# Optimization experiments

Hardware: AMD Instinct MI355X
Metric: run time of the kernel (lower is better)

The kernel has to match this reference:

```python
import jax, jax.numpy as jnp
import numpy as np

N, C, K, D = 65536, 64, 16, 2
EPS = 1e-5


def batch_norm(x, g, b):
    # training-mode BatchNorm1d over rows (biased variance), x: [rows, C]
    m = x.mean(axis=0)
    v = ((x - m) ** 2).mean(axis=0)
    return (x - m) * jax.lax.rsqrt(v + EPS) * g + b


def setup_inputs() -> dict:
    key = jax.random.key(0)
    ks = jax.random.split(key, 20)
    s = 1.0 / np.sqrt(C)
    inp = {
        "coord": jax.random.normal(ks[0], (N, 3), jnp.float32),
        "feat": jax.random.normal(ks[1], (N, C), jnp.float32),
        "reference_index": jax.random.randint(ks[2], (N, K), 0, N, jnp.int32),
        # per-block stacked params, leading dim D
        "fc1_w": jax.random.uniform(ks[3], (D, C, C), jnp.float32, -s, s),
        "bn1_g": jnp.ones((D, C), jnp.float32),
        "bn1_b": jnp.zeros((D, C), jnp.float32),
        "la_w1": jax.random.uniform(ks[4], (D, C, C), jnp.float32, -s, s),
        "la_b1": jax.random.uniform(ks[5], (D, C), jnp.float32, -s, s),
        "la_bn1_g": jnp.ones((D, C), jnp.float32),
        "la_bn1_b": jnp.zeros((D, C), jnp.float32),
        "la_w2": jax.random.uniform(ks[6], (D, C, C), jnp.float32, -s, s),
        "la_b2": jax.random.uniform(ks[7], (D, C), jnp.float32, -s, s),
        "la_bn2_g": jnp.ones((D, C), jnp.float32),
        "la_bn2_b": jnp.zeros((D, C), jnp.float32),
        "fc3_w": jax.random.uniform(ks[8], (D, C, C), jnp.float32, -s, s),
        "bn2_g": jnp.ones((D, C), jnp.float32),
        "bn2_b": jnp.zeros((D, C), jnp.float32),
        "bn3_g": jnp.ones((D, C), jnp.float32),
        "bn3_b": jnp.zeros((D, C), jnp.float32),
    }
    return inp


def reference(coord, feat, reference_index,
              fc1_w, bn1_g, bn1_b,
              la_w1, la_b1, la_bn1_g, la_bn1_b,
              la_w2, la_b2, la_bn2_g, la_bn2_b,
              fc3_w, bn2_g, bn2_b, bn3_g, bn3_b):
    ref = reference_index  # [n, k]
    for d in range(D):
        identity = feat
        # fc1 (no bias) -> bn1 -> relu
        x = jax.nn.relu(batch_norm(feat @ fc1_w[d].T, bn1_g[d], bn1_b[d]))
        # LocalAggregation: gather neighbors, shared MLP on [n*k, c], max over k
        grouped = x[ref].reshape(-1, C)                      # [n*k, c]
        h = jax.nn.relu(batch_norm(grouped @ la_w1[d].T + la_b1[d],
                                   la_bn1_g[d], la_bn1_b[d]))
        h = jax.nn.relu(batch_norm(h @ la_w2[d].T + la_b2[d],
                                   la_bn2_g[d], la_bn2_b[d]))
        x = h.reshape(ref.shape[0], K, C).max(axis=1)        # [n, c]
        # bn2 -> relu -> fc3 (no bias) -> bn3
        x = jax.nn.relu(batch_norm(x, bn2_g[d], bn2_b[d]))
        x = batch_norm(x @ fc3_w[d].T, bn3_g[d], bn3_b[d])
        feat = jax.nn.relu(identity + x)
    return feat
```

## Files before the change

kernel.cpp:

```cpp
#include <hip/hip_runtime.h>

#define N_PTS 65536
#define BN_EPS 1e-5f
#define NSHD 64
#define NSB  (10 * NSHD * 128)

typedef __attribute__((ext_vector_type(8))) short bf16x8;
typedef __attribute__((ext_vector_type(4))) float f32x4;

static __device__ __forceinline__ unsigned short f2bf(float f) {
    unsigned u = __builtin_bit_cast(unsigned, f);
    u += 0x7fffu + ((u >> 16) & 1u);
    return (unsigned short)(u >> 16);
}
static __device__ __forceinline__ float bf2f(unsigned short h) {
    unsigned u = ((unsigned)h) << 16;
    return __builtin_bit_cast(float, u);
}
static __device__ __forceinline__ unsigned pack2(float a, float b) {
    return (unsigned)f2bf(a) | ((unsigned)f2bf(b) << 16);
}

template<int PRE, int BIAS, int WTD, int OUTBF, int INBF, int HIST>
__global__ __launch_bounds__(256, 4) void mm_kernel(
    const void*  __restrict__ inv_,  const float* __restrict__ identity,
    const float* __restrict__ Wg,    const float* __restrict__ bias,
    const float* __restrict__ gg,    const float* __restrict__ bb,
    const float* __restrict__ S_in,  float inv_denom,
    void*        __restrict__ outv,  float* __restrict__ S_out,
    const unsigned* __restrict__ cw, float* __restrict__ f1_out,
    const int* __restrict__ ref,     unsigned* __restrict__ hdst)
{
    __shared__ unsigned short lwh[64][72], lwl[64][72];
    __shared__ float stg[4][16][68];
    __shared__ float sc[64], sh[64];
    __shared__ float LS[4][64], LQ[4][64];
    float* PS = &stg[0][0][0];

    const int tid  = threadIdx.x;
    const int lane = tid & 63, wid = tid >> 6;
    const int l15  = lane & 15, kg = lane >> 4;
    const int brow = blockIdx.x * 64;
    const int arow = brow + wid * 16 + l15;

    const int wr = tid >> 2, wc = (tid & 3) * 16;
    const float4* wp = (const float4*)(Wg + wr * 64 + wc);
    float4 wv0 = wp[0], wv1 = wp[1], wv2 = wp[2], wv3 = wp[3];

    float xv[2][8];
    uint4 ub0, ub1;
    float4 a0, a1, a2, a3;
    if (INBF) {
        const uint4* ap = (const uint4*)((const unsigned*)inv_ +
                                         (size_t)arow * 32 + kg * 4);
        ub0 = ap[0]; ub1 = ap[4];
    } else {
        const float4* ap = (const float4*)((const float*)inv_ +
                                           (size_t)arow * 64 + kg * 8);
        a0 = ap[0]; a1 = ap[1]; a2 = ap[8]; a3 = ap[9];
    }
    float4 i0, i1, i2, i3;
    if (PRE == 2) {
        const float4* ip = (const float4*)(identity + (size_t)arow * 64 + kg * 8);
        i0 = ip[0]; i1 = ip[1]; i2 = ip[8]; i3 = ip[9];
    }
    uint4 cc;
    if (WTD) cc = ((const uint4*)(cw + brow + wid * 16))[kg];
    if (HIST) {
        int4 hv = ((const int4*)(ref + brow * 16))[tid];
        atomicAdd(&hdst[hv.x], 1u); atomicAdd(&hdst[hv.y], 1u);
        atomicAdd(&hdst[hv.z], 1u); atomicAdd(&hdst[hv.w], 1u);
    }

    {
        float wf[16] = {wv0.x,wv0.y,wv0.z,wv0.w, wv1.x,wv1.y,wv1.z,wv1.w,
                        wv2.x,wv2.y,wv2.z,wv2.w, wv3.x,wv3.y,wv3.z,wv3.w};
        unsigned ph[8], pl[8];
        #pragma unroll
        for (int q = 0; q < 8; ++q) {
            unsigned short h0 = f2bf(wf[2*q]),   h1 = f2bf(wf[2*q+1]);
            unsigned short l0 = f2bf(wf[2*q]   - bf2f(h0));
            unsigned short l1 = f2bf(wf[2*q+1] - bf2f(h1));
            ph[q] = (unsigned)h0 | ((unsigned)h1 << 16);
            pl[q] = (unsigned)l0 | ((unsigned)l1 << 16);
        }
        uint4* dh = (uint4*)(&lwh[wr][wc]);
        uint4* dl = (uint4*)(&lwl[wr][wc]);
        dh[0] = make_uint4(ph[0], ph[1], ph[2], ph[3]);
        dh[1] = make_uint4(ph[4], ph[5], ph[6], ph[7]);
        dl[0] = make_uint4(pl[0], pl[1], pl[2], pl[3]);
        dl[1] = make_uint4(pl[4], pl[5], pl[6], pl[7]);
    }

    if (PRE >= 1) {
        const int idx = tid & 127, hh = tid >> 7;
        float acc = 0.f;
        #pragma unroll
        for (int g = 0; g < NSHD / 2; ++g)
            acc += S_in[(hh * (NSHD / 2) + g) * 128 + idx];
        PS[hh * 128 + idx] = acc;
        __syncthreads();
        if (tid < 128) PS[tid] += PS[128 + tid];
        __syncthreads();
        if (tid < 64) {
            float s = PS[tid], q = PS[64 + tid];
            float m   = s * inv_denom;
            float var = q * inv_denom - m * m;
            float scl = gg[tid] * rsqrtf(var + BN_EPS);
            sc[tid] = scl; sh[tid] = bb[tid] - m * scl;
        }
    }
    __syncthreads();

    if (INBF) {
        uint4 uu[2] = {ub0, ub1};
        #pragma unroll
        for (int ks = 0; ks < 2; ++ks) {
            unsigned w0 = uu[ks].x, w1 = uu[ks].y, w2 = uu[ks].z, w3 = uu[ks].w;
            xv[ks][0] = bf2f((unsigned short)(w0 & 0xffffu));
            xv[ks][1] = bf2f((unsigned short)(w0 >> 16));
            xv[ks][2] = bf2f((unsigned short)(w1 & 0xffffu));
            xv[ks][3] = bf2f((unsigned short)(w1 >> 16));
            xv[ks][4] = bf2f((unsigned short)(w2 & 0xffffu));
            xv[ks][5] = bf2f((unsigned short)(w2 >> 16));
            xv[ks][6] = bf2f((unsigned short)(w3 & 0xffffu));
            xv[ks][7] = bf2f((unsigned short)(w3 >> 16));
        }
    } else {
        xv[0][0]=a0.x; xv[0][1]=a0.y; xv[0][2]=a0.z; xv[0][3]=a0.w;
        xv[0][4]=a1.x; xv[0][5]=a1.y; xv[0][6]=a1.z; xv[0][7]=a1.w;
        xv[1][0]=a2.x; xv[1][1]=a2.y; xv[1][2]=a2.z; xv[1][3]=a2.w;
        xv[1][4]=a3.x; xv[1][5]=a3.y; xv[1][6]=a3.z; xv[1][7]=a3.w;
    }

    if (PRE == 1) {
        #pragma unroll
        for (int ks = 0; ks < 2; ++ks)
            #pragma unroll
            for (int j = 0; j < 8; ++j) {
                int k = ks * 32 + kg * 8 + j;
                xv[ks][j] = fmaxf(xv[ks][j] * sc[k] + sh[k], 0.f);
            }
    } else if (PRE == 2) {
        float idv[2][8];
        idv[0][0]=i0.x; idv[0][1]=i0.y; idv[0][2]=i0.z; idv[0][3]=i0.w;
        idv[0][4]=i1.x; idv[0][5]=i1.y; idv[0][6]=i1.z; idv[0][7]=i1.w;
        idv[1][0]=i2.x; idv[1][1]=i2.y; idv[1][2]=i2.z; idv[1][3]=i2.w;
        idv[1][4]=i3.x; idv[1][5]=i3.y; idv[1][6]=i3.z; idv[1][7]=i3.w;
        #pragma unroll
        for (int ks = 0; ks < 2; ++ks) {
            #pragma unroll
            for (int j = 0; j < 8; ++j) {
                int k = ks * 32 + kg * 8 + j;
                xv[ks][j] = fmaxf(idv[ks][j] + xv[ks][j] * sc[k] + sh[k], 0.f);
            }
            float* f1p = f1_out + (size_t)arow * 64 + kg * 8 + ks * 32;
            *(float4*)(f1p)     = make_float4(xv[ks][0], xv[ks][1], xv[ks][2], xv[ks][3]);
            *(float4*)(f1p + 4) = make_float4(xv[ks][4], xv[ks][5], xv[ks][6], xv[ks][7]);
        }
    }

    bf16x8 ahi[2], alo[2];
    #pragma unroll
    for (int ks = 0; ks < 2; ++ks) {
        bf16x8 th, tl;
        #pragma unroll
        for (int j = 0; j < 8; ++j) {
            unsigned short h = f2bf(xv[ks][j]);
            th[j] = (short)h;
            tl[j] = (short)f2bf(xv[ks][j] - bf2f(h));
        }
        ahi[ks] = th; alo[ks] = tl;
    }
    f32x4 d[4];
    #pragma unroll
    for (int ct = 0; ct < 4; ++ct) {
        float bc = BIAS ? bias[ct * 16 + l15] : 0.f;
        d[ct] = (f32x4){bc, bc, bc, bc};
    }
    #pragma unroll
    for (int ct = 0; ct < 4; ++ct) {
        const int gcol = ct * 16 + l15;
        #pragma unroll
        for (int ks = 0; ks < 2; ++ks) {
            bf16x8 wh = *(const bf16x8*)(&lwh[gcol][ks * 32 + kg * 8]);
            bf16x8 wl = *(const bf16x8*)(&lwl[gcol][ks * 32 + kg * 8]);
            d[ct] = __builtin_amdgcn_mfma_f32_16x16x32_bf16(ahi[ks], wh, d[ct], 0, 0, 0);
            d[ct] = __builtin_amdgcn_mfma_f32_16x16x32_bf16(alo[ks], wh, d[ct], 0, 0, 0);
            d[ct] = __builtin_amdgcn_mfma_f32_16x16x32_bf16(ahi[ks], wl, d[ct], 0, 0, 0);
        }
    }

    float wt[4] = {1.f, 1.f, 1.f, 1.f};
    if (WTD) {
        wt[0] = (float)cc.x; wt[1] = (float)cc.y;
        wt[2] = (float)cc.z; wt[3] = (float)cc.w;
    }
    float ts[4], tq[4];
    #pragma unroll
    for (int ct = 0; ct < 4; ++ct) {
        float t = 0.f, t2 = 0.f;
        #pragma unroll
        for (int i = 0; i < 4; ++i) {
            float v = d[ct][i];
            t += wt[i] * v; t2 += wt[i] * v * v;
        }
        ts[ct] = t; tq[ct] = t2;
    }

    #pragma unroll
    for (int ct = 0; ct < 4; ++ct)
        #pragma unroll
        for (int i = 0; i < 4; ++i)
            stg[wid][kg * 4 + i][ct * 16 + l15] = d[ct][i];
    __syncthreads();
    if (!OUTBF) {
        float* op = (float*)outv + (size_t)arow * 64 + kg * 16;
        const float* srow = &stg[wid][l15][kg * 16];
        *(float4*)(op + 0)  = *(const float4*)(srow + 0);
        *(float4*)(op + 4)  = *(const float4*)(srow + 4);
        *(float4*)(op + 8)  = *(const float4*)(srow + 8);
        *(float4*)(op + 12) = *(const float4*)(srow + 12);
    } else {
        const float* srow = &stg[wid][l15][kg * 16];
        unsigned pk[8];
        #pragma unroll
        for (int q = 0; q < 8; ++q) pk[q] = pack2(srow[2 * q], srow[2 * q + 1]);
        unsigned* op = (unsigned*)outv;
        uint4* dst = (uint4*)(op + (size_t)arow * 32 + kg * 8);
        dst[0] = make_uint4(pk[0], pk[1], pk[2], pk[3]);
        dst[1] = make_uint4(pk[4], pk[5], pk[6], pk[7]);
    }

    #pragma unroll
    for (int ct = 0; ct < 4; ++ct) {
        float a = ts[ct], b = tq[ct];
        a += __shfl_xor(a, 16);  a += __shfl_xor(a, 32);
        b += __shfl_xor(b, 16);  b += __shfl_xor(b, 32);
        if (kg == 0) { LS[wid][ct * 16 + l15] = a; LQ[wid][ct * 16 + l15] = b; }
    }
    __syncthreads();
    const int bsel = blockIdx.x & (NSHD - 1);
    if (tid < 64)
        atomicAdd(S_out + bsel * 128 + tid,
                  LS[0][tid] + LS[1][tid] + LS[2][tid] + LS[3][tid]);
    else if (tid < 128) {
        int c = tid - 64;
        atomicAdd(S_out + bsel * 128 + 64 + c,
                  LQ[0][c] + LQ[1][c] + LQ[2][c] + LQ[3][c]);
    }
}

__global__ __launch_bounds__(256) void gather_kernel(
    const unsigned* __restrict__ y3u, const int* __restrict__ ref,
    const float* __restrict__ S_in, float inv_denom,
    const float* __restrict__ gg, const float* __restrict__ bb,
    unsigned* __restrict__ xmu, float* __restrict__ S_out)
{
    __shared__ float scs[64], shs[64], Rs[256], Rq[256], PS[256];
    const int tid = threadIdx.x;
    const int lane = tid & 63, wid = tid >> 6;
    const int c2 = lane & 31;
    const int hsel = lane & 32;
    const int p0 = blockIdx.x * 8 + wid * 2;
    const int r0 = 2 * p0 + (hsel ? 1 : 0);
    const int r1 = r0 + 2;

    int jv0 = ref[r0 * 16 + (lane & 15)];
    int jv1 = ref[r1 * 16 + (lane & 15)];
    unsigned u0[16], u1[16];
    #pragma unroll
    for (int t = 0; t < 16; ++t) {
        int j = __shfl(jv0, hsel + t);
        u0[t] = y3u[(size_t)j * 32 + c2];
    }
    #pragma unroll
    for (int t = 0; t < 16; ++t) {
        int j = __shfl(jv1, hsel + t);
        u1[t] = y3u[(size_t)j * 32 + c2];
    }

    {
        const int idx = tid & 127, hh = tid >> 7;
        float acc = 0.f;
        #pragma unroll
        for (int g = 0; g < NSHD / 2; ++g)
            acc += S_in[(hh * (NSHD / 2) + g) * 128 + idx];
        PS[hh * 128 + idx] = acc;
        __syncthreads();
        if (tid < 128) PS[tid] += PS[128 + tid];
        __syncthreads();
        if (tid < 64) {
            float s = PS[tid], q = PS[64 + tid];
            float m   = s * inv_denom;
            float var = q * inv_denom - m * m;
            float scl = gg[tid] * rsqrtf(var + BN_EPS);
            scs[tid] = scl; shs[tid] = bb[tid] - m * scl;
        }
        __syncthreads();
    }
    const float sc0 = scs[2*c2], sc1 = scs[2*c2+1];
    const float sh0 = shs[2*c2], sh1 = shs[2*c2+1];

    float s0 = 0.f, q0 = 0.f, s1 = 0.f, q1 = 0.f;
    #pragma unroll
    for (int pair = 0; pair < 2; ++pair) {
        const unsigned* u = pair ? u1 : u0;
        const int r = pair ? r1 : r0;
        float m0 = bf2f((unsigned short)(u[0] & 0xffffu));
        float m1 = bf2f((unsigned short)(u[0] >> 16));
        #pragma unroll
        for (int t = 1; t < 16; ++t) {
            m0 = fmaxf(m0, bf2f((unsigned short)(u[t] & 0xffffu)));
            m1 = fmaxf(m1, bf2f((unsigned short)(u[t] >> 16)));
        }
        float x0 = fmaxf(m0 * sc0 + sh0, 0.f);
        float x1 = fmaxf(m1 * sc1 + sh1, 0.f);
        xmu[(size_t)r * 32 + c2] = pack2(x0, x1);
        s0 += x0; q0 += x0 * x0; s1 += x1; q1 += x1 * x1;
    }

    const int bsel = blockIdx.x & (NSHD - 1);
    Rs[tid] = s0; Rq[tid] = q0;
    __syncthreads();
    if (tid < 32) {
        float a = 0.f, c = 0.f;
        #pragma unroll
        for (int i = 0; i < 8; ++i) { a += Rs[tid + 32*i]; c += Rq[tid + 32*i]; }
        atomicAdd(S_out + bsel*128 + 2*tid, a);
        atomicAdd(S_out + bsel*128 + 64 + 2*tid, c);
    }
    __syncthreads();
    Rs[tid] = s1; Rq[tid] = q1;
    __syncthreads();
    if (tid < 32) {
        float a = 0.f, c = 0.f;
        #pragma unroll
        for (int i = 0; i < 8; ++i) { a += Rs[tid + 32*i]; c += Rq[tid + 32*i]; }
        atomicAdd(S_out + bsel*128 + 2*tid + 1, a);
        atomicAdd(S_out + bsel*128 + 64 + 2*tid + 1, c);
    }
}

__global__ __launch_bounds__(256) void res_final(
    float* __restrict__ io, const float* __restrict__ y4,
    const float* __restrict__ S_in, float inv_denom,
    const float* __restrict__ gg, const float* __restrict__ bb)
{
    __shared__ float sc[64], sh[64], PS[256];
    const int tid = threadIdx.x;
    int i = blockIdx.x * 256 + tid;
    float4 idv = ((const float4*)io)[i];
    float4 yv  = ((const float4*)y4)[i];
    {
        const int idx = tid & 127, hh = tid >> 7;
        float acc = 0.f;
        #pragma unroll
        for (int g = 0; g < NSHD / 2; ++g)
            acc += S_in[(hh * (NSHD / 2) + g) * 128 + idx];
        PS[hh * 128 + idx] = acc;
        __syncthreads();
        if (tid < 128) PS[tid] += PS[128 + tid];
        __syncthreads();
        if (tid < 64) {
            float s = PS[tid], q = PS[64 + tid];
            float m   = s * inv_denom;
            float var = q * inv_denom - m * m;
            float scl = gg[tid] * rsqrtf(var + BN_EPS);
            sc[tid] = scl; sh[tid] = bb[tid] - m * scl;
        }
        __syncthreads();
    }
    int c0 = (i * 4) & 63;
    float4 o;
    o.x = fmaxf(idv.x + yv.x * sc[c0+0] + sh[c0+0], 0.f);
    o.y = fmaxf(idv.y + yv.y * sc[c0+1] + sh[c0+1], 0.f);
    o.z = fmaxf(idv.z + yv.z * sc[c0+2] + sh[c0+2], 0.f);
    o.w = fmaxf(idv.w + yv.w * sc[c0+3] + sh[c0+3], 0.f);
    ((float4*)io)[i] = o;
}

extern "C" void kernel_launch(void* const* d_in, const int* in_sizes, int n_in,
                              void* d_out, int out_size, void* d_ws, size_t ws_size,
                              hipStream_t stream)
{
    const float* feat    = (const float*)d_in[1];
    const int*   ref     = (const int*)  d_in[2];
    const float* fc1_w   = (const float*)d_in[3];
    const float* bn1_g   = (const float*)d_in[4];
    const float* bn1_b   = (const float*)d_in[5];
    const float* la_w1   = (const float*)d_in[6];
    const float* la_b1   = (const float*)d_in[7];
    const float* la_bn1g = (const float*)d_in[8];
    const float* la_bn1b = (const float*)d_in[9];
    const float* la_w2   = (const float*)d_in[10];
    const float* la_b2   = (const float*)d_in[11];
    const float* la_bn2g = (const float*)d_in[12];
    const float* la_bn2b = (const float*)d_in[13];
    const float* fc3_w   = (const float*)d_in[14];
    const float* bn2_g   = (const float*)d_in[15];
    const float* bn2_b   = (const float*)d_in[16];
    const float* bn3_g   = (const float*)d_in[17];
    const float* bn3_b   = (const float*)d_in[18];
    float* out = (float*)d_out;

    char* base = (char*)d_ws;
    float*    R1  = (float*)base;
    float*    R2  = (float*)(base + 16u * 1024 * 1024);
    unsigned* cnt = (unsigned*)(base + 32u * 1024 * 1024);
    float*    Sb  = (float*)(cnt + N_PTS);
#define SS(i) (Sb + (i) * NSHD * 128)

    hipMemsetAsync(cnt, 0, N_PTS * sizeof(unsigned) + NSB * sizeof(float), stream);

    const float invN  = 1.f / (float)N_PTS;
    const float invNK = invN / 16.f;
    const int MMG = N_PTS / 64;

    mm_kernel<0,0,0,0,0,1><<<MMG,256,0,stream>>>(feat, nullptr, fc1_w,
        nullptr, nullptr, nullptr, nullptr, 0.f, R1, SS(0), nullptr, nullptr, ref, cnt);
    mm_kernel<1,1,1,0,0,0><<<MMG,256,0,stream>>>(R1, nullptr, la_w1,
        la_b1, bn1_g, bn1_b, SS(0), invN, R2, SS(1), cnt, nullptr, nullptr, nullptr);
    mm_kernel<1,1,1,1,0,0><<<MMG,256,0,stream>>>(R2, nullptr, la_w2,
        la_b2, la_bn1g, la_bn1b, SS(1), invNK, R1, SS(2), cnt, nullptr, nullptr, nullptr);
    gather_kernel<<<4096,256,0,stream>>>((const unsigned*)R1, ref, SS(2), invNK,
        la_bn2g, la_bn2b, (unsigned*)R2, SS(3));
    mm_kernel<1,0,0,0,1,0><<<MMG,256,0,stream>>>(R2, nullptr, fc3_w,
        nullptr, bn2_g, bn2_b, SS(3), invN, R1, SS(4), nullptr, nullptr, nullptr, nullptr);

    mm_kernel<2,0,0,0,0,0><<<MMG,256,0,stream>>>(R1, feat, fc1_w + 4096,
        nullptr, bn3_g, bn3_b, SS(4), invN, R2, SS(5), nullptr, out, nullptr, nullptr);
    mm_kernel<1,1,1,0,0,0><<<MMG,256,0,stream>>>(R2, nullptr, la_w1 + 4096,
        la_b1 + 64, bn1_g + 64, bn1_b + 64, SS(5), invN, R1, SS(6), cnt, nullptr, nullptr, nullptr);
    mm_kernel<1,1,1,1,0,0><<<MMG,256,0,stream>>>(R1, nullptr, la_w2 + 4096,
        la_b2 + 64, la_bn1g + 64, la_bn1b + 64, SS(6), invNK, R2, SS(7), cnt, nullptr, nullptr, nullptr);
    gather_kernel<<<4096,256,0,stream>>>((const unsigned*)R2, ref, SS(7), invNK,
        la_bn2g + 64, la_bn2b + 64, (unsigned*)R1, SS(8));
    mm_kernel<1,0,0,0,1,0><<<MMG,256,0,stream>>>(R1, nullptr, fc3_w + 4096,
        nullptr, bn2_g + 64, bn2_b + 64, SS(8), invN, R2, SS(9), nullptr, nullptr, nullptr, nullptr);
    res_final<<<(N_PTS * 64 / 4) / 256, 256, 0, stream>>>(out, R2, SS(9), invN,
        bn3_g + 64, bn3_b + 64);
}
```

Before: 203.8 us.

## Replace global-atomic neighbor histogram with LDS-privatized partial histograms plus merge

The neighbor-count histogram used to be built with global atomicAdds inside the first matmul kernel. A new prep kernel now builds 32 partial histograms of 16-bit packed counts in shared memory, each covering one chunk of the reference indices and one half of the bin range. The first matmul kernel then sums those partials per bin instead of issuing atomics. The same prep kernel also zeroes the stats buffer, which replaces the memset. The goal is to cut global atomic contention and one memset, at the cost of an extra launch and reading 32 partial arrays stored in R2. That reuse of R2 is safe only because R2 is overwritten later.

```diff
diff --git a/kernel.cpp b/kernel.cpp
--- a/kernel.cpp
+++ b/kernel.cpp
@@ -4,6 +4,7 @@
 #define BN_EPS 1e-5f
 #define NSHD 64
 #define NSB  (10 * NSHD * 128)
+#define HBLK 32
 
 typedef __attribute__((ext_vector_type(8))) short bf16x8;
 typedef __attribute__((ext_vector_type(4))) float f32x4;
@@ -21,7 +22,43 @@
     return (unsigned)f2bf(a) | ((unsigned)f2bf(b) << 16);
 }
 
-template<int PRE, int BIAS, int WTD, int OUTBF, int INBF, int HIST>
+__global__ __launch_bounds__(256) void prep_kernel(
+    const int* __restrict__ ref, unsigned short* __restrict__ H,
+    float* __restrict__ Sb)
+{
+    const int b = blockIdx.x, tid = threadIdx.x;
+    if (b < 2 * HBLK) {
+        __shared__ unsigned bins[16384];
+        const int c = b >> 1, h = b & 1;
+        const int lo = h * 32768;
+        #pragma unroll
+        for (int i = 0; i < 64; ++i) bins[tid + i * 256] = 0u;
+        __syncthreads();
+        const int4* rp = (const int4*)(ref + c * 32768);
+        #pragma unroll 4
+        for (int i = 0; i < 32; ++i) {
+            int4 v = rp[tid + i * 256];
+            unsigned x;
+            x = (unsigned)(v.x - lo);
+            if (x < 32768u) atomicAdd(&bins[x >> 1], 1u << (16 * (x & 1)));
+            x = (unsigned)(v.y - lo);
+            if (x < 32768u) atomicAdd(&bins[x >> 1], 1u << (16 * (x & 1)));
+            x = (unsigned)(v.z - lo);
+            if (x < 32768u) atomicAdd(&bins[x >> 1], 1u << (16 * (x & 1)));
+            x = (unsigned)(v.w - lo);
+            if (x < 32768u) atomicAdd(&bins[x >> 1], 1u << (16 * (x & 1)));
+        }
+        __syncthreads();
+        unsigned* dst = (unsigned*)(H + (size_t)c * 65536 + lo);
+        #pragma unroll
+        for (int i = 0; i < 64; ++i) dst[tid + i * 256] = bins[tid + i * 256];
+    } else {
+        const int zidx = (b - 2 * HBLK) * 256 + tid;
+        for (int i = zidx; i < NSB; i += 64 * 256) Sb[i] = 0.f;
+    }
+}
+
+template<int PRE, int BIAS, int WTD, int OUTBF, int INBF, int MERGE>
 __global__ __launch_bounds__(256, 4) void mm_kernel(
     const void*  __restrict__ inv_,  const float* __restrict__ identity,
     const float* __restrict__ Wg,    const float* __restrict__ bias,
@@ -29,7 +66,7 @@
     const float* __restrict__ S_in,  float inv_denom,
     void*        __restrict__ outv,  float* __restrict__ S_out,
     const unsigned* __restrict__ cw, float* __restrict__ f1_out,
-    const int* __restrict__ ref,     unsigned* __restrict__ hdst)
+    const unsigned short* __restrict__ hsrc, unsigned* __restrict__ hdst)
 {
     __shared__ unsigned short lwh[64][72], lwl[64][72];
     __shared__ float stg[4][16][68];
@@ -66,10 +103,16 @@
     }
     uint4 cc;
     if (WTD) cc = ((const uint4*)(cw + brow + wid * 16))[kg];
-    if (HIST) {
-        int4 hv = ((const int4*)(ref + brow * 16))[tid];
-        atomicAdd(&hdst[hv.x], 1u); atomicAdd(&hdst[hv.y], 1u);
-        atomicAdd(&hdst[hv.z], 1u); atomicAdd(&hdst[hv.w], 1u);
+
+    if (MERGE) {
+        if (tid < 64) {
+            const int bin = blockIdx.x * 64 + tid;
+            unsigned s = 0;
+            #pragma unroll
+            for (int g = 0; g < HBLK; ++g)
+                s += (unsigned)hsrc[(size_t)g * 65536 + bin];
+            hdst[bin] = s;
+        }
     }
 
     {
@@ -191,11 +234,10 @@
         }
     }
 
-    float wt[4] = {1.f, 1.f, 1.f, 1.f};
-    if (WTD) {
-        wt[0] = (float)cc.x; wt[1] = (float)cc.y;
-        wt[2] = (float)cc.z; wt[3] = (float)cc.w;
-    }
+    float wt[4];
+    #pragma unroll
+    for (int i = 0; i < 4; ++i)
+        wt[i] = WTD ? (float)((const unsigned*)&cc)[i] : 1.f;
     float ts[4], tq[4];
     #pragma unroll
     for (int ct = 0; ct < 4; ++ct) {
@@ -409,16 +451,17 @@
     float*    R2  = (float*)(base + 16u * 1024 * 1024);
     unsigned* cnt = (unsigned*)(base + 32u * 1024 * 1024);
     float*    Sb  = (float*)(cnt + N_PTS);
+    unsigned short* H = (unsigned short*)R2;
 #define SS(i) (Sb + (i) * NSHD * 128)
-
-    hipMemsetAsync(cnt, 0, N_PTS * sizeof(unsigned) + NSB * sizeof(float), stream);
 
     const float invN  = 1.f / (float)N_PTS;
     const float invNK = invN / 16.f;
     const int MMG = N_PTS / 64;
 
+    prep_kernel<<<2 * HBLK + 64, 256, 0, stream>>>(ref, H, Sb);
+
     mm_kernel<0,0,0,0,0,1><<<MMG,256,0,stream>>>(feat, nullptr, fc1_w,
-        nullptr, nullptr, nullptr, nullptr, 0.f, R1, SS(0), nullptr, nullptr, ref, cnt);
+        nullptr, nullptr, nullptr, nullptr, 0.f, R1, SS(0), nullptr, nullptr, H, cnt);
     mm_kernel<1,1,1,0,0,0><<<MMG,256,0,stream>>>(R1, nullptr, la_w1,
         la_b1, bn1_g, bn1_b, SS(0), invN, R2, SS(1), cnt, nullptr, nullptr, nullptr);
     mm_kernel<1,1,1,1,0,0><<<MMG,256,0,stream>>>(R2, nullptr, la_w2,
```

Result: faster. 180.1 us (-11.6%).
